# Optimization experiments

Hardware: AMD Instinct MI355X
Metric: run time of the kernel (lower is better)

Reference implementation:

```python
import jax, jax.numpy as jnp
import numpy as np

B, CIN, H, W = 8, 1, 192, 192
COUT, KH, KW = 8, 7, 7


def setup_inputs() -> dict:
    key = jax.random.key(0)
    k1, k2, k3 = jax.random.split(key, 3)
    x = jax.random.normal(k1, (B, CIN, H, W), dtype=jnp.float32)
    # original init: filter ~ N(0, 0.01), alpha = 0 (use small nonzero alpha)
    filt = 0.01 * jax.random.normal(k2, (COUT, CIN, KH, KW), dtype=jnp.float32)
    alpha = 0.1 * jax.random.normal(k3, (COUT, CIN), dtype=jnp.float32)
    return {"x": x, "filt": filt, "alpha": alpha}


def _smorph(x, filt, alpha):
    # x: [B, Cin, H, W]; filt: [Cout, Cin, kh, kw]; alpha: [Cout, Cin]
    b, cin, h, w = x.shape
    cout, _, kh, kw = filt.shape
    ho, wo = h - kh + 1, w - kw + 1  # 'valid' windowing as in _smorph_py
    # sliding-window patches: [B, Cin, kh*kw, Ho, Wo] (static slices, traced once)
    patches = jnp.stack(
        [x[:, :, ky:ky + ho, kx:kx + wo] for ky in range(kh) for kx in range(kw)],
        axis=2,
    )
    # s[b,co,ci,k,y,x] = input[b,ci,y+ky,x+kx] + filter[co,ci,ky,kx]
    s = patches[:, None] + filt.reshape(cout, cin, kh * kw, 1, 1)[None]
    a = alpha[None, :, :, None, None, None]  # broadcast over B, taps, space
    e = jnp.exp(a * s)
    num = jnp.sum(s * e, axis=(2, 3))  # sum over Cin and taps -> [B,Cout,Ho,Wo]
    den = jnp.sum(e, axis=(2, 3))
    return num / den


def reference(x, filt, alpha):
    # dual=False: single soft-morphology pass
    return _smorph(x, filt, alpha)
```

## Files before the change

kernel.cpp:

```cpp
#include <hip/hip_runtime.h>

#ifndef __has_builtin
#define __has_builtin(x) 0
#endif

constexpr int B_    = 8;
constexpr int H_    = 192;
constexpr int W_    = 192;
constexpr int COUT_ = 8;
constexpr int KH_   = 7;
constexpr int KW_   = 7;
constexpr int HO_   = H_ - KH_ + 1;
constexpr int WO_   = W_ - KW_ + 1;

__device__ __forceinline__ float fast_exp2(float v) {
#if __has_builtin(__builtin_amdgcn_exp2f)
    return __builtin_amdgcn_exp2f(v);
#else
    return exp2f(v);
#endif
}

__global__ __launch_bounds__(256) void smorph_kernel(
    const float* __restrict__ x,
    const float* __restrict__ filt,
    const float* __restrict__ alpha,
    float* __restrict__ out)
{
    const int ox = blockIdx.x * 32 + threadIdx.x;
    const int oy = blockIdx.y * 8  + threadIdx.y;
    const int b  = blockIdx.z;
    if (ox >= WO_ || oy >= HO_) return;

    const float* xb = x + b * (H_ * W_);

    float win[KH_ * KW_];
#pragma unroll
    for (int ky = 0; ky < KH_; ++ky) {
#pragma unroll
        for (int kx = 0; kx < KW_; ++kx) {
            win[ky * KW_ + kx] = xb[(oy + ky) * W_ + (ox + kx)];
        }
    }

    constexpr float LOG2E = 1.44269504088896340736f;

#pragma unroll 1
    for (int c = 0; c < COUT_; ++c) {
        const float a   = alpha[c];
        const float al2 = a * LOG2E;
        float num = 0.0f;
        float den = 0.0f;
#pragma unroll
        for (int k = 0; k < KH_ * KW_; ++k) {
            const float f = filt[c * (KH_ * KW_) + k];
            const float s = win[k] + f;
            const float e = fast_exp2(al2 * s);
            num = __builtin_fmaf(s, e, num);
            den += e;
        }
        out[((b * COUT_ + c) * HO_ + oy) * WO_ + ox] = num / den;
    }
}

extern "C" void kernel_launch(void* const* d_in, const int* in_sizes, int n_in,
                              void* d_out, int out_size, void* d_ws, size_t ws_size,
                              hipStream_t stream) {
    const float* x     = (const float*)d_in[0];
    const float* filt  = (const float*)d_in[1];
    const float* alpha = (const float*)d_in[2];
    float* out = (float*)d_out;

    dim3 block(32, 8, 1);
    dim3 grid((WO_ + 31) / 32, (HO_ + 7) / 8, B_);
    smorph_kernel<<<grid, block, 0, stream>>>(x, filt, alpha, out);
}
```

Measured before the change: 82.24 us.

## Factor exp(a(x+f)) into input and filter terms with shared-memory tiling

The kernel rewrites exp(a*(x+f)) as exp(a*x)*exp(a*f). The filter factors F and F*f are precomputed once in a small setup kernel. The main kernel computes exp(a*x) and x*exp(a*x) once per input pixel per channel into an LDS tile, and each thread produces two adjacent outputs using only FMAs. This removes the 49 exponentials per output per channel that dominated the old kernel. In exchange it adds an extra kernel launch, workspace use, per-channel block barriers, and a product form that could lose accuracy for larger alpha.

```diff
diff --git a/kernel.cpp b/kernel.cpp
--- a/kernel.cpp
+++ b/kernel.cpp
@@ -3,6 +3,21 @@
 #ifndef __has_builtin
 #define __has_builtin(x) 0
 #endif
+
+__device__ __forceinline__ float fexp2(float v) {
+#if __has_builtin(__builtin_amdgcn_exp2f)
+    return __builtin_amdgcn_exp2f(v);
+#else
+    return exp2f(v);
+#endif
+}
+__device__ __forceinline__ float frcp(float v) {
+#if __has_builtin(__builtin_amdgcn_rcpf)
+    return __builtin_amdgcn_rcpf(v);
+#else
+    return 1.0f / v;
+#endif
+}
 
 constexpr int B_    = 8;
 constexpr int H_    = 192;
@@ -12,54 +27,101 @@
 constexpr int KW_   = 7;
 constexpr int HO_   = H_ - KH_ + 1;
 constexpr int WO_   = W_ - KW_ + 1;
+constexpr float LOG2E = 1.44269504088896340736f;
 
-__device__ __forceinline__ float fast_exp2(float v) {
-#if __has_builtin(__builtin_amdgcn_exp2f)
-    return __builtin_amdgcn_exp2f(v);
-#else
-    return exp2f(v);
-#endif
+constexpr int TX   = 64;
+constexpr int TY   = 8;
+constexpr int IX   = TX + KW_ - 1;
+constexpr int IY   = TY + KH_ - 1;
+constexpr int NPIX = IX * IY;
+
+__global__ void smorph_setup(const float* __restrict__ filt,
+                             const float* __restrict__ alpha,
+                             float* __restrict__ ws) {
+    for (int i = threadIdx.x; i < COUT_ * KH_ * KW_; i += 256) {
+        int c = i / 49, r = i - c * 49, ky = r / 7, kx = r - ky * 7;
+        float a2 = alpha[c] * LOG2E;
+        float f  = filt[c * 49 + ky * 7 + kx];
+        float F  = fexp2(a2 * f);
+        ws[c * 56 + ky * 8 + kx]       = F;
+        ws[448 + c * 56 + ky * 8 + kx] = F * f;
+    }
 }
 
-__global__ __launch_bounds__(256) void smorph_kernel(
+__global__ __launch_bounds__(256) void smorph_main(
     const float* __restrict__ x,
-    const float* __restrict__ filt,
     const float* __restrict__ alpha,
+    const float* __restrict__ fg,
     float* __restrict__ out)
 {
-    const int ox = blockIdx.x * 32 + threadIdx.x;
-    const int oy = blockIdx.y * 8  + threadIdx.y;
-    const int b  = blockIdx.z;
-    if (ox >= WO_ || oy >= HO_) return;
+    __shared__ __align__(16) float2 PH[IY * IX];
+
+    const int tx = threadIdx.x;
+    const int ty = threadIdx.y;
+    const int tid = ty * 32 + tx;
+    const int bx0 = blockIdx.x * TX;
+    const int by0 = blockIdx.y * TY;
+    const int b   = blockIdx.z;
 
     const float* xb = x + b * (H_ * W_);
-
-    float win[KH_ * KW_];
-#pragma unroll
-    for (int ky = 0; ky < KH_; ++ky) {
-#pragma unroll
-        for (int kx = 0; kx < KW_; ++kx) {
-            win[ky * KW_ + kx] = xb[(oy + ky) * W_ + (ox + kx)];
-        }
+    const float* sptr[4];
+    int sidx[4];
+    int scnt = 0;
+    for (int i = tid; i < NPIX; i += 256) {
+        int iy = i / IX, ix = i - iy * IX;
+        int gy = min(by0 + iy, H_ - 1);
+        int gx = min(bx0 + ix, W_ - 1);
+        sptr[scnt] = xb + gy * W_ + gx;
+        sidx[scnt] = i;
+        ++scnt;
     }
 
-    constexpr float LOG2E = 1.44269504088896340736f;
+    const int ox = bx0 + 2 * tx;
+    const int oy = by0 + ty;
+    const bool valid = (ox + 1 < WO_) && (oy < HO_);
 
 #pragma unroll 1
     for (int c = 0; c < COUT_; ++c) {
-        const float a   = alpha[c];
-        const float al2 = a * LOG2E;
-        float num = 0.0f;
-        float den = 0.0f;
+        const float a2 = alpha[c] * LOG2E;
+
+        for (int j = 0; j < scnt; ++j) {
+            float xv = *sptr[j];
+            float P  = fexp2(a2 * xv);
+            PH[sidx[j]] = make_float2(P, xv * P);
+        }
+        __syncthreads();
+
+        float num0 = 0.f, den0 = 0.f, num1 = 0.f, den1 = 0.f;
 #pragma unroll
-        for (int k = 0; k < KH_ * KW_; ++k) {
-            const float f = filt[c * (KH_ * KW_) + k];
-            const float s = win[k] + f;
-            const float e = fast_exp2(al2 * s);
-            num = __builtin_fmaf(s, e, num);
-            den += e;
+        for (int ky = 0; ky < KH_; ++ky) {
+            float Fk[7], Gk[7];
+#pragma unroll
+            for (int j = 0; j < 7; ++j) {
+                Fk[j] = fg[c * 56 + ky * 8 + j];
+                Gk[j] = fg[448 + c * 56 + ky * 8 + j];
+            }
+            const float4* rp = (const float4*)&PH[(ty + ky) * IX + 2 * tx];
+            float4 q0 = rp[0], q1 = rp[1], q2 = rp[2], q3 = rp[3];
+            float P[8] = {q0.x, q0.z, q1.x, q1.z, q2.x, q2.z, q3.x, q3.z};
+            float Hh[8] = {q0.y, q0.w, q1.y, q1.w, q2.y, q2.w, q3.y, q3.w};
+#pragma unroll
+            for (int kx = 0; kx < 7; ++kx) {
+                num0 = fmaf(Fk[kx], Hh[kx], num0);
+                num0 = fmaf(Gk[kx], P[kx], num0);
+                den0 = fmaf(Fk[kx], P[kx], den0);
+                num1 = fmaf(Fk[kx], Hh[kx + 1], num1);
+                num1 = fmaf(Gk[kx], P[kx + 1], num1);
+                den1 = fmaf(Fk[kx], P[kx + 1], den1);
+            }
         }
-        out[((b * COUT_ + c) * HO_ + oy) * WO_ + ox] = num / den;
+
+        if (valid) {
+            float2 o;
+            o.x = num0 * frcp(den0);
+            o.y = num1 * frcp(den1);
+            *(float2*)&out[((b * COUT_ + c) * HO_ + oy) * WO_ + ox] = o;
+        }
+        __syncthreads();
     }
 }
 
@@ -70,8 +132,11 @@
     const float* filt  = (const float*)d_in[1];
     const float* alpha = (const float*)d_in[2];
     float* out = (float*)d_out;
+    float* ws  = (float*)d_ws;
+
+    smorph_setup<<<1, 256, 0, stream>>>(filt, alpha, ws);
 
     dim3 block(32, 8, 1);
-    dim3 grid((WO_ + 31) / 32, (HO_ + 7) / 8, B_);
-    smorph_kernel<<<grid, block, 0, stream>>>(x, filt, alpha, out);
+    dim3 grid((WO_ + TX - 1) / TX, (HO_ + TY - 1) / TY, B_);
+    smorph_main<<<grid, block, 0, stream>>>(x, alpha, ws, out);
 }
```

Measured after the change: 86.18 us. 4.8% more time.
